# Optimization experiments

Hardware: AMD Instinct MI355X
Metric: run time of the kernel (lower is better)

## Reference

```python
import jax, jax.numpy as jnp
import numpy as np

DM, NE, ES, ESZ = 1024, 16, 4, 64  # dm, nexperts, expertsets, expertsize (dff = NE*ES*ESZ = 4096)
BATCH, SEQ = 8, 2048


def setup_inputs() -> dict:
    key = jax.random.key(0)
    k = jax.random.split(key, 5)
    scale = 0.02
    return {
        "x": jax.random.normal(k[0], (BATCH, SEQ, DM), dtype=jnp.float32),
        "controller": jax.random.normal(k[1], (DM, NE, ES), dtype=jnp.float32) * scale,
        "f1": jax.random.normal(k[2], (DM, NE, ES, ESZ), dtype=jnp.float32) * scale,
        "f2": jax.random.normal(k[3], (NE, ES, ESZ, DM), dtype=jnp.float32) * scale,
        "bias": jax.random.normal(k[4], (NE, ES, ESZ), dtype=jnp.float32) * scale,
    }


def reference(x, controller, f1, f2, bias):
    ne = controller.shape[1]
    d = x.shape[-1]
    # group tokens: [..., (b t), d] -> [..., b, t, d] with t = nexperts
    grouped = x.reshape(x.shape[:-2] + (-1, ne, d))
    # controller logits per token/expert/expertset: [..., b, t, e, s]
    logits = jnp.einsum('...btd,des->...btes', grouped, controller)
    # deterministic tiebreaker over the token-within-group axis t
    tie = jnp.linspace(0.0, 1e-6, ne, dtype=logits.dtype).reshape(ne, 1, 1)
    logits = logits + tie
    # hard top-1 permutation: for each (e, s) pick the argmax token t (one-hot over t)
    perm = (logits == jnp.max(logits, axis=-3, keepdims=True)).astype(x.dtype)
    # dispatch: select the chosen token's activations per (e, s): [..., b, e, s, d]
    sel = jnp.einsum('...btd,...btes->...besd', grouped, perm)
    # expert FFN up-projection + bias + relu: [..., b, e, s, f]
    inner = jax.nn.relu(jnp.einsum('...besd,desf->...besf', sel, f1) + bias)
    # expert FFN down-projection: [..., b, e, s, d]
    inter = jnp.einsum('...besf,esfd->...besd', inner, f2)
    # un-permute back to token positions: [..., b, t, d]
    out = jnp.einsum('...besd,...btes->...btd', inter, perm)
    return out.reshape(x.shape)
```

## Files before the change

kernel.cpp:

```cpp
#include <hip/hip_runtime.h>

#define DM   1024
#define NES  64
#define ESZ  64
#define NG   1024
#define TOK  16

typedef __bf16 bf16;
typedef __bf16 bf16x4 __attribute__((ext_vector_type(4)));
typedef __bf16 bf16x8 __attribute__((ext_vector_type(8)));
typedef float  f32x4  __attribute__((ext_vector_type(4)));

__device__ __forceinline__ void gld_lds16(const bf16* g, bf16* s) {
    __builtin_amdgcn_global_load_lds(
        (const __attribute__((address_space(1))) void*)g,
        (__attribute__((address_space(3))) void*)s, 16, 0, 0);
}

__global__ __launch_bounds__(256) void k0_transpose(const float* __restrict__ f1,
                                                    const float* __restrict__ f2,
                                                    bf16* __restrict__ f1p,
                                                    bf16* __restrict__ f2t) {
    __shared__ float tile[64 * 65];
    const int es = blockIdx.y, d0 = blockIdx.x * 64, tid = threadIdx.x;
    #pragma unroll
    for (int i = 0; i < 4; ++i) {
        int idx = i * 256 + tid; int r = idx >> 4, c4 = (idx & 15) * 4;
        float4 v = *(const float4*)(f1 + (size_t)(d0 + r) * 4096 + es * 64 + c4);
        tile[r * 65 + c4] = v.x; tile[r * 65 + c4 + 1] = v.y;
        tile[r * 65 + c4 + 2] = v.z; tile[r * 65 + c4 + 3] = v.w;
    }
    __syncthreads();
    #pragma unroll
    for (int i = 0; i < 2; ++i) {
        int idx = i * 256 + tid; int f = idx >> 3, dl0 = (idx & 7) * 8;
        bf16x8 o;
        #pragma unroll
        for (int j = 0; j < 8; ++j) o[j] = (bf16)tile[(dl0 + j) * 65 + f];
        *(bf16x8*)(f1p + (size_t)es * 65536 + f * 1024 + d0 + dl0) = o;
    }
    __syncthreads();
    #pragma unroll
    for (int i = 0; i < 4; ++i) {
        int idx = i * 256 + tid; int r = idx >> 4, c4 = (idx & 15) * 4;
        float4 v = *(const float4*)(f2 + (size_t)es * 65536 + r * 1024 + d0 + c4);
        tile[r * 65 + c4] = v.x; tile[r * 65 + c4 + 1] = v.y;
        tile[r * 65 + c4 + 2] = v.z; tile[r * 65 + c4 + 3] = v.w;
    }
    __syncthreads();
    #pragma unroll
    for (int i = 0; i < 2; ++i) {
        int idx = i * 256 + tid; int dl = idx >> 3, f0 = (idx & 7) * 8;
        bf16x8 o;
        #pragma unroll
        for (int j = 0; j < 8; ++j) o[j] = (bf16)tile[(f0 + j) * 65 + dl];
        *(bf16x8*)(f2t + (size_t)es * 65536 + (size_t)(d0 + dl) * 64 + f0) = o;
    }
}

__global__ __launch_bounds__(256) void k1_logits(const float* __restrict__ x,
                                                 const float* __restrict__ ctrl,
                                                 int* __restrict__ sel,
                                                 unsigned* __restrict__ selp) {
    __shared__ __align__(16) float xs[TOK * 132];
    __shared__ float sl[TOK * NES];
    __shared__ int   st[NES];
    const int bg  = blockIdx.x;
    const int tid = threadIdx.x;
    const int es  = tid & 63;
    const int tq  = tid >> 6;
    const float* xg = x + (size_t)bg * (TOK * DM);
    const float* cp = ctrl + es;
    float acc[4] = {0.f, 0.f, 0.f, 0.f};
    for (int d0 = 0; d0 < DM; d0 += 128) {
        __syncthreads();
        #pragma unroll
        for (int c = 0; c < 2; ++c) {
            int idx = tid + c * 256;
            int tr  = idx >> 5;
            int c4  = (idx & 31) * 4;
            float4 v = *(const float4*)(xg + tr * DM + d0 + c4);
            *(float4*)(xs + tr * 132 + c4) = v;
        }
        __syncthreads();
        #pragma unroll 2
        for (int dl4 = 0; dl4 < 128; dl4 += 4) {
            float4 v0 = *(const float4*)(xs + (tq * 4 + 0) * 132 + dl4);
            float4 v1 = *(const float4*)(xs + (tq * 4 + 1) * 132 + dl4);
            float4 v2 = *(const float4*)(xs + (tq * 4 + 2) * 132 + dl4);
            float4 v3 = *(const float4*)(xs + (tq * 4 + 3) * 132 + dl4);
            float c0 = cp[(size_t)(d0 + dl4 + 0) * 64];
            float c1 = cp[(size_t)(d0 + dl4 + 1) * 64];
            float c2 = cp[(size_t)(d0 + dl4 + 2) * 64];
            float c3 = cp[(size_t)(d0 + dl4 + 3) * 64];
            acc[0] += v0.x * c0; acc[1] += v1.x * c0;
            acc[2] += v2.x * c0; acc[3] += v3.x * c0;
            acc[0] += v0.y * c1; acc[1] += v1.y * c1;
            acc[2] += v2.y * c1; acc[3] += v3.y * c1;
            acc[0] += v0.z * c2; acc[1] += v1.z * c2;
            acc[2] += v2.z * c2; acc[3] += v3.z * c2;
            acc[0] += v0.w * c3; acc[1] += v1.w * c3;
            acc[2] += v2.w * c3; acc[3] += v3.w * c3;
        }
    }
    #pragma unroll
    for (int i = 0; i < 4; ++i) {
        int t = tq * 4 + i;
        sl[t * NES + es] = acc[i] + (float)t * (1e-6f / 15.f);
    }
    __syncthreads();
    if (tid < NES) {
        float best = -1e30f; int bi = 0;
        #pragma unroll
        for (int t = 0; t < TOK; ++t) {
            float v = sl[t * NES + tid];
            if (v >= best) { best = v; bi = t; }
        }
        sel[bg * NES + tid] = bi;
        st[tid] = bi;
    }
    __syncthreads();
    if (tid < 8) {
        unsigned p = 0;
        #pragma unroll
        for (int k = 0; k < 8; ++k) p |= (unsigned)st[tid * 8 + k] << (4 * k);
        selp[bg * 8 + tid] = p;
    }
}

__global__ __launch_bounds__(256) void k2_ffn1(const float* __restrict__ x,
                                               const bf16* __restrict__ f1p,
                                               const float* __restrict__ bias,
                                               const int* __restrict__ sel,
                                               bf16* __restrict__ inner) {
    __shared__ int  sel_s[128];
    __shared__ __align__(16) bf16 As[128 * 40];
    __shared__ __align__(16) bf16 Bs[64 * 40];
    const int es  = blockIdx.y;
    const int g0  = blockIdx.x * 128;
    const int tid = threadIdx.x;
    if (tid < 128) sel_s[tid] = sel[(g0 + tid) * 64 + es];
    __syncthreads();

    const int w = tid >> 6, l = tid & 63, quad = l >> 4, lr = l & 15;
    int tokrow[4];
    #pragma unroll
    for (int p = 0; p < 4; ++p) {
        int grow = p * 32 + (tid >> 3);
        tokrow[p] = (g0 + grow) * 16 + sel_s[grow];
    }
    const int c4 = (tid & 7) * 4;
    const int bf = tid >> 2, bd = (tid & 3) * 8;
    const bf16* f1es = f1p + (size_t)es * (DM * ESZ);

    f32x4 acc[2][4];
    #pragma unroll
    for (int mt = 0; mt < 2; ++mt)
        #pragma unroll
        for (int nt = 0; nt < 4; ++nt)
            acc[mt][nt] = (f32x4){0.f, 0.f, 0.f, 0.f};

    for (int k0 = 0; k0 < DM; k0 += 32) {
        #pragma unroll
        for (int p = 0; p < 4; ++p) {
            int grow = p * 32 + (tid >> 3);
            float4 v = *(const float4*)(x + (size_t)tokrow[p] * DM + k0 + c4);
            bf16x4 ob = {(bf16)v.x, (bf16)v.y, (bf16)v.z, (bf16)v.w};
            *(bf16x4*)(As + grow * 40 + c4) = ob;
        }
        {
            bf16x8 v = *(const bf16x8*)(f1es + bf * 1024 + k0 + bd);
            *(bf16x8*)(Bs + bf * 40 + bd) = v;
        }
        __syncthreads();
        bf16x8 av[2], bv[4];
        #pragma unroll
        for (int mt = 0; mt < 2; ++mt)
            av[mt] = *(const bf16x8*)(As + (w * 32 + mt * 16 + lr) * 40 + quad * 8);
        #pragma unroll
        for (int nt = 0; nt < 4; ++nt)
            bv[nt] = *(const bf16x8*)(Bs + (nt * 16 + lr) * 40 + quad * 8);
        #pragma unroll
        for (int mt = 0; mt < 2; ++mt)
            #pragma unroll
            for (int nt = 0; nt < 4; ++nt)
                acc[mt][nt] = __builtin_amdgcn_mfma_f32_16x16x32_bf16(
                    av[mt], bv[nt], acc[mt][nt], 0, 0, 0);
        __syncthreads();
    }
    bf16* innes = inner + (size_t)es * (NG * ESZ);
    #pragma unroll
    for (int mt = 0; mt < 2; ++mt)
        #pragma unroll
        for (int nt = 0; nt < 4; ++nt) {
            int f = nt * 16 + lr;
            float b = bias[es * 64 + f];
            #pragma unroll
            for (int r = 0; r < 4; ++r) {
                int grow = w * 32 + mt * 16 + quad * 4 + r;
                float v = acc[mt][nt][r] + b;
                v = v > 0.f ? v : 0.f;
                innes[(size_t)(g0 + grow) * 64 + f] = (bf16)v;
            }
        }
}

__global__ __launch_bounds__(256) void k3_ffn2(const bf16* __restrict__ inner,
                                               const bf16* __restrict__ f2t,
                                               const unsigned* __restrict__ selp,
                                               float* __restrict__ out) {
    __shared__ float accs[512 * 32];
    __shared__ __align__(16) bf16 As[2][32 * 64];
    __shared__ __align__(16) bf16 Bs[2][32 * 64];
    const int d0  = blockIdx.x * 32;
    const int g0  = blockIdx.y * 32;
    const int tid = threadIdx.x;
    const int w = tid >> 6, l = tid & 63, quad = l >> 4, lr = l & 15;
    const int mh = w >> 1, nh = w & 1;

    unsigned sp[4][8];
    #pragma unroll
    for (int r = 0; r < 4; ++r) {
        int gl = mh * 16 + quad * 4 + r;
        uint4 a = *(const uint4*)(selp + (size_t)(g0 + gl) * 8);
        uint4 b = *(const uint4*)(selp + (size_t)(g0 + gl) * 8 + 4);
        sp[r][0] = a.x; sp[r][1] = a.y; sp[r][2] = a.z; sp[r][3] = a.w;
        sp[r][4] = b.x; sp[r][5] = b.y; sp[r][6] = b.z; sp[r][7] = b.w;
    }

    const int srow = tid >> 3;
    const int scb  = ((tid & 7) * 16) ^ ((srow & 7) << 4);
    const bf16* srcA = inner + (size_t)(g0 + srow) * 64 + (scb >> 1);
    const bf16* srcB = f2t   + (size_t)(d0 + srow) * 64 + (scb >> 1);
    bf16* dA0 = &As[0][w * 512]; bf16* dA1 = &As[1][w * 512];
    bf16* dB0 = &Bs[0][w * 512]; bf16* dB1 = &Bs[1][w * 512];

    #pragma unroll
    for (int i = 0; i < 16; ++i)
        ((f32x4*)accs)[i * 256 + tid] = (f32x4){0.f, 0.f, 0.f, 0.f};

    gld_lds16(srcA, dA0);
    gld_lds16(srcB, dB0);
    __syncthreads();

    const int rowA = mh * 16 + lr, rowB = nh * 16 + lr;
    const int offA0 = rowA * 128 + ((quad * 16)      ^ ((rowA & 7) << 4));
    const int offA1 = rowA * 128 + ((quad * 16 + 64) ^ ((rowA & 7) << 4));
    const int offB0 = rowB * 128 + ((quad * 16)      ^ ((rowB & 7) << 4));
    const int offB1 = rowB * 128 + ((quad * 16 + 64) ^ ((rowB & 7) << 4));

    #pragma unroll
    for (int es = 0; es < 64; ++es) {
        const int cur = es & 1;
        if (es < 63) {
            if (cur == 0) { gld_lds16(srcA + (size_t)(es + 1) * 65536, dA1);
                            gld_lds16(srcB + (size_t)(es + 1) * 65536, dB1); }
            else          { gld_lds16(srcA + (size_t)(es + 1) * 65536, dA0);
                            gld_lds16(srcB + (size_t)(es + 1) * 65536, dB0); }
            asm volatile("s_waitcnt vmcnt(2)" ::: "memory");
        } else {
            asm volatile("s_waitcnt vmcnt(0)" ::: "memory");
        }
        asm volatile("s_barrier" ::: "memory");

        const char* a = (const char*)As[cur];
        const char* b = (const char*)Bs[cur];
        bf16x8 a0 = *(const bf16x8*)(a + offA0);
        bf16x8 a1 = *(const bf16x8*)(a + offA1);
        bf16x8 b0 = *(const bf16x8*)(b + offB0);
        bf16x8 b1 = *(const bf16x8*)(b + offB1);
        f32x4 z = {0.f, 0.f, 0.f, 0.f};
        z = __builtin_amdgcn_mfma_f32_16x16x32_bf16(a0, b0, z, 0, 0, 0);
        z = __builtin_amdgcn_mfma_f32_16x16x32_bf16(a1, b1, z, 0, 0, 0);

        const int dw = es >> 3, sh = (es & 7) * 4;
        #pragma unroll
        for (int r = 0; r < 4; ++r) {
            int t    = (sp[r][dw] >> sh) & 15;
            int gl   = mh * 16 + quad * 4 + r;
            int scol = (nh * 16 + lr) ^ ((t & 7) << 2);
            accs[(gl * 16 + t) * 32 + scol] += z[r];
        }
        asm volatile("s_barrier" ::: "memory");
    }
    __syncthreads();
    #pragma unroll
    for (int i = 0; i < 16; ++i) {
        int fi = i * 256 + tid;
        int row = fi >> 3, q = fi & 7;
        int scol4 = (q * 4) ^ ((row & 7) << 2);
        f32x4 v = *(f32x4*)(accs + row * 32 + scol4);
        __builtin_nontemporal_store(v, (f32x4*)(out + (size_t)(g0 * 16 + row) * DM + d0 + q * 4));
    }
}

extern "C" void kernel_launch(void* const* d_in, const int* in_sizes, int n_in,
                              void* d_out, int out_size, void* d_ws, size_t ws_size,
                              hipStream_t stream) {
    const float* x    = (const float*)d_in[0];
    const float* ctrl = (const float*)d_in[1];
    const float* f1   = (const float*)d_in[2];
    const float* f2   = (const float*)d_in[3];
    const float* bias = (const float*)d_in[4];
    float* out = (float*)d_out;

    char* ws = (char*)d_ws;
    bf16*     f1p   = (bf16*)(ws);
    bf16*     f2t   = (bf16*)(ws + 8388608);
    bf16*     inner = (bf16*)(ws + 16777216);
    int*      sel   = (int*)(ws + 25165824);
    unsigned* selp  = (unsigned*)(ws + 25427968);

    hipLaunchKernelGGL(k0_transpose, dim3(16, 64), dim3(256), 0, stream, f1, f2, f1p, f2t);
    hipLaunchKernelGGL(k1_logits,    dim3(1024),   dim3(256), 0, stream, x, ctrl, sel, selp);
    hipLaunchKernelGGL(k2_ffn1,      dim3(8, 64),  dim3(256), 0, stream, x, f1p, bias, sel, inner);
    hipLaunchKernelGGL(k3_ffn2,      dim3(32, 32), dim3(256), 0, stream, inner, f2t, selp, out);
}
```

Before: 306.1 us.

## Emit bf16 x copy from logits kernel, stage controller in LDS, prefetch ffn1 tiles

The logits kernel now stages controller chunks in shared memory instead of issuing strided global loads per thread. It prefetches the next x and controller chunk into registers while computing the current one. When the workspace is large enough, it also writes a bf16 copy of x, so the ffn1 gather reads half the bytes and skips conversion. The ffn1 kernel switches to 64-row tiles with register prefetch of the next k-slice, doubling the grid. This adds an extra 32MB write in k1 and depends on workspace size.

```diff
diff --git a/kernel.cpp b/kernel.cpp
--- a/kernel.cpp
+++ b/kernel.cpp
@@ -58,11 +58,14 @@
     }
 }
 
+template<int WRITE_XB>
 __global__ __launch_bounds__(256) void k1_logits(const float* __restrict__ x,
                                                  const float* __restrict__ ctrl,
                                                  int* __restrict__ sel,
-                                                 unsigned* __restrict__ selp) {
-    __shared__ __align__(16) float xs[TOK * 132];
+                                                 unsigned* __restrict__ selp,
+                                                 bf16* __restrict__ xb) {
+    __shared__ __align__(16) float xs[TOK * 64];
+    __shared__ __align__(16) float cs[64 * 64];
     __shared__ float sl[TOK * NES];
     __shared__ int   st[NES];
     const int bg  = blockIdx.x;
@@ -70,29 +73,45 @@
     const int es  = tid & 63;
     const int tq  = tid >> 6;
     const float* xg = x + (size_t)bg * (TOK * DM);
-    const float* cp = ctrl + es;
+    const int xr = tid >> 4, xc = (tid & 15) * 4;
     float acc[4] = {0.f, 0.f, 0.f, 0.f};
-    for (int d0 = 0; d0 < DM; d0 += 128) {
+
+    float4 xv;
+    float4 cv[4];
+    xv = *(const float4*)(xg + xr * DM + xc);
+    #pragma unroll
+    for (int j = 0; j < 4; ++j)
+        cv[j] = *(const float4*)(ctrl + (size_t)(tid + j * 256) * 4);
+
+    for (int c = 0; c < 16; ++c) {
+        const int d0 = c * 64;
         __syncthreads();
-        #pragma unroll
-        for (int c = 0; c < 2; ++c) {
-            int idx = tid + c * 256;
-            int tr  = idx >> 5;
-            int c4  = (idx & 31) * 4;
-            float4 v = *(const float4*)(xg + tr * DM + d0 + c4);
-            *(float4*)(xs + tr * 132 + c4) = v;
-        }
+        *(float4*)(xs + xr * 64 + xc) = xv;
+        if (WRITE_XB) {
+            bf16x4 o = {(bf16)xv.x, (bf16)xv.y, (bf16)xv.z, (bf16)xv.w};
+            *(bf16x4*)(xb + (size_t)(bg * TOK + xr) * DM + d0 + xc) = o;
+        }
+        #pragma unroll
+        for (int j = 0; j < 4; ++j)
+            *(float4*)(cs + tid * 4 + j * 1024) = cv[j];
         __syncthreads();
-        #pragma unroll 2
-        for (int dl4 = 0; dl4 < 128; dl4 += 4) {
-            float4 v0 = *(const float4*)(xs + (tq * 4 + 0) * 132 + dl4);
-            float4 v1 = *(const float4*)(xs + (tq * 4 + 1) * 132 + dl4);
-            float4 v2 = *(const float4*)(xs + (tq * 4 + 2) * 132 + dl4);
-            float4 v3 = *(const float4*)(xs + (tq * 4 + 3) * 132 + dl4);
-            float c0 = cp[(size_t)(d0 + dl4 + 0) * 64];
-            float c1 = cp[(size_t)(d0 + dl4 + 1) * 64];
-            float c2 = cp[(size_t)(d0 + dl4 + 2) * 64];
-            float c3 = cp[(size_t)(d0 + dl4 + 3) * 64];
+        if (c < 15) {
+            xv = *(const float4*)(xg + xr * DM + d0 + 64 + xc);
+            #pragma unroll
+            for (int j = 0; j < 4; ++j)
+                cv[j] = *(const float4*)(ctrl + (size_t)(d0 + 64) * 64 +
+                                         (size_t)(tid + j * 256) * 4);
+        }
+        #pragma unroll
+        for (int dl4 = 0; dl4 < 64; dl4 += 4) {
+            float4 v0 = *(const float4*)(xs + (tq * 4 + 0) * 64 + dl4);
+            float4 v1 = *(const float4*)(xs + (tq * 4 + 1) * 64 + dl4);
+            float4 v2 = *(const float4*)(xs + (tq * 4 + 2) * 64 + dl4);
+            float4 v3 = *(const float4*)(xs + (tq * 4 + 3) * 64 + dl4);
+            float c0 = cs[(dl4 + 0) * 64 + es];
+            float c1 = cs[(dl4 + 1) * 64 + es];
+            float c2 = cs[(dl4 + 2) * 64 + es];
+            float c3 = cs[(dl4 + 3) * 64 + es];
             acc[0] += v0.x * c0; acc[1] += v1.x * c0;
             acc[2] += v2.x * c0; acc[3] += v3.x * c0;
             acc[0] += v0.y * c1; acc[1] += v1.y * c1;
@@ -128,81 +147,92 @@
     }
 }
 
+template<int USE_XB>
 __global__ __launch_bounds__(256) void k2_ffn1(const float* __restrict__ x,
+                                               const bf16* __restrict__ xb,
                                                const bf16* __restrict__ f1p,
                                                const float* __restrict__ bias,
                                                const int* __restrict__ sel,
                                                bf16* __restrict__ inner) {
-    __shared__ int  sel_s[128];
-    __shared__ __align__(16) bf16 As[128 * 40];
+    __shared__ int  sel_s[64];
+    __shared__ __align__(16) bf16 As[64 * 40];
     __shared__ __align__(16) bf16 Bs[64 * 40];
     const int es  = blockIdx.y;
-    const int g0  = blockIdx.x * 128;
+    const int g0  = blockIdx.x * 64;
     const int tid = threadIdx.x;
-    if (tid < 128) sel_s[tid] = sel[(g0 + tid) * 64 + es];
+    if (tid < 64) sel_s[tid] = sel[(size_t)(g0 + tid) * 64 + es];
     __syncthreads();
 
     const int w = tid >> 6, l = tid & 63, quad = l >> 4, lr = l & 15;
-    int tokrow[4];
-    #pragma unroll
-    for (int p = 0; p < 4; ++p) {
-        int grow = p * 32 + (tid >> 3);
-        tokrow[p] = (g0 + grow) * 16 + sel_s[grow];
-    }
-    const int c4 = (tid & 7) * 4;
-    const int bf = tid >> 2, bd = (tid & 3) * 8;
+    const int rowq = tid >> 2, colq = (tid & 3) * 8;
+    const int row8 = tid >> 3, c4 = (tid & 7) * 4;
     const bf16* f1es = f1p + (size_t)es * (DM * ESZ);
 
-    f32x4 acc[2][4];
-    #pragma unroll
-    for (int mt = 0; mt < 2; ++mt)
-        #pragma unroll
-        for (int nt = 0; nt < 4; ++nt)
-            acc[mt][nt] = (f32x4){0.f, 0.f, 0.f, 0.f};
+    int tokq = 0, tok0 = 0, tok1 = 0;
+    if (USE_XB) {
+        tokq = (g0 + rowq) * 16 + sel_s[rowq];
+    } else {
+        tok0 = (g0 + row8) * 16 + sel_s[row8];
+        tok1 = (g0 + 32 + row8) * 16 + sel_s[32 + row8];
+    }
+
+    bf16x8 ra, rb;
+    float4 r0, r1;
+    if (USE_XB) {
+        ra = *(const bf16x8*)(xb + (size_t)tokq * DM + colq);
+    } else {
+        r0 = *(const float4*)(x + (size_t)tok0 * DM + c4);
+        r1 = *(const float4*)(x + (size_t)tok1 * DM + c4);
+    }
+    rb = *(const bf16x8*)(f1es + rowq * 1024 + colq);
+
+    f32x4 acc[4];
+    #pragma unroll
+    for (int nt = 0; nt < 4; ++nt) acc[nt] = (f32x4){0.f, 0.f, 0.f, 0.f};
 
     for (int k0 = 0; k0 < DM; k0 += 32) {
-        #pragma unroll
-        for (int p = 0; p < 4; ++p) {
-            int grow = p * 32 + (tid >> 3);
-            float4 v = *(const float4*)(x + (size_t)tokrow[p] * DM + k0 + c4);
-            bf16x4 ob = {(bf16)v.x, (bf16)v.y, (bf16)v.z, (bf16)v.w};
-            *(bf16x4*)(As + grow * 40 + c4) = ob;
-        }
-        {
-            bf16x8 v = *(const bf16x8*)(f1es + bf * 1024 + k0 + bd);
-            *(bf16x8*)(Bs + bf * 40 + bd) = v;
-        }
+        if (USE_XB) {
+            *(bf16x8*)(As + rowq * 40 + colq) = ra;
+        } else {
+            bf16x4 o0 = {(bf16)r0.x, (bf16)r0.y, (bf16)r0.z, (bf16)r0.w};
+            bf16x4 o1 = {(bf16)r1.x, (bf16)r1.y, (bf16)r1.z, (bf16)r1.w};
+            *(bf16x4*)(As + row8 * 40 + c4) = o0;
+            *(bf16x4*)(As + (32 + row8) * 40 + c4) = o1;
+        }
+        *(bf16x8*)(Bs + rowq * 40 + colq) = rb;
         __syncthreads();
-        bf16x8 av[2], bv[4];
-        #pragma unroll
-        for (int mt = 0; mt < 2; ++mt)
-            av[mt] = *(const bf16x8*)(As + (w * 32 + mt * 16 + lr) * 40 + quad * 8);
+        if (k0 + 32 < DM) {
+            if (USE_XB) {
+                ra = *(const bf16x8*)(xb + (size_t)tokq * DM + k0 + 32 + colq);
+            } else {
+                r0 = *(const float4*)(x + (size_t)tok0 * DM + k0 + 32 + c4);
+                r1 = *(const float4*)(x + (size_t)tok1 * DM + k0 + 32 + c4);
+            }
+            rb = *(const bf16x8*)(f1es + rowq * 1024 + k0 + 32 + colq);
+        }
+        bf16x8 av = *(const bf16x8*)(As + (w * 16 + lr) * 40 + quad * 8);
+        bf16x8 bv[4];
         #pragma unroll
         for (int nt = 0; nt < 4; ++nt)
             bv[nt] = *(const bf16x8*)(Bs + (nt * 16 + lr) * 40 + quad * 8);
         #pragma unroll
-        for (int mt = 0; mt < 2; ++mt)
-            #pragma unroll
-            for (int nt = 0; nt < 4; ++nt)
-                acc[mt][nt] = __builtin_amdgcn_mfma_f32_16x16x32_bf16(
-                    av[mt], bv[nt], acc[mt][nt], 0, 0, 0);
+        for (int nt = 0; nt < 4; ++nt)
+            acc[nt] = __builtin_amdgcn_mfma_f32_16x16x32_bf16(av, bv[nt], acc[nt], 0, 0, 0);
         __syncthreads();
     }
     bf16* innes = inner + (size_t)es * (NG * ESZ);
     #pragma unroll
-    for (int mt = 0; mt < 2; ++mt)
-        #pragma unroll
-        for (int nt = 0; nt < 4; ++nt) {
-            int f = nt * 16 + lr;
-            float b = bias[es * 64 + f];
-            #pragma unroll
-            for (int r = 0; r < 4; ++r) {
-                int grow = w * 32 + mt * 16 + quad * 4 + r;
-                float v = acc[mt][nt][r] + b;
-                v = v > 0.f ? v : 0.f;
-                innes[(size_t)(g0 + grow) * 64 + f] = (bf16)v;
-            }
-        }
+    for (int nt = 0; nt < 4; ++nt) {
+        int f = nt * 16 + lr;
+        float b = bias[es * 64 + f];
+        #pragma unroll
+        for (int r = 0; r < 4; ++r) {
+            int grow = w * 16 + quad * 4 + r;
+            float v = acc[nt][r] + b;
+            v = v > 0.f ? v : 0.f;
+            innes[(size_t)(g0 + grow) * 64 + f] = (bf16)v;
+        }
+    }
 }
 
 __global__ __launch_bounds__(256) void k3_ffn2(const bf16* __restrict__ inner,
@@ -310,9 +340,18 @@
     bf16*     inner = (bf16*)(ws + 16777216);
     int*      sel   = (int*)(ws + 25165824);
     unsigned* selp  = (unsigned*)(ws + 25427968);
+    bf16*     xb    = (bf16*)(ws + 25460736);
+
+    const size_t need_xb = (size_t)25460736 + (size_t)NG * TOK * DM * sizeof(bf16);
+    const bool use_xb = ws_size >= need_xb;
 
     hipLaunchKernelGGL(k0_transpose, dim3(16, 64), dim3(256), 0, stream, f1, f2, f1p, f2t);
-    hipLaunchKernelGGL(k1_logits,    dim3(1024),   dim3(256), 0, stream, x, ctrl, sel, selp);
-    hipLaunchKernelGGL(k2_ffn1,      dim3(8, 64),  dim3(256), 0, stream, x, f1p, bias, sel, inner);
-    hipLaunchKernelGGL(k3_ffn2,      dim3(32, 32), dim3(256), 0, stream, inner, f2t, selp, out);
-}
+    if (use_xb) {
+        hipLaunchKernelGGL((k1_logits<1>), dim3(1024), dim3(256), 0, stream, x, ctrl, sel, selp, xb);
+        hipLaunchKernelGGL((k2_ffn1<1>),   dim3(16, 64), dim3(256), 0, stream, x, xb, f1p, bias, sel, inner);
+    } else {
+        hipLaunchKernelGGL((k1_logits<0>), dim3(1024), dim3(256), 0, stream, x, ctrl, sel, selp, xb);
+        hipLaunchKernelGGL((k2_ffn1<0>),   dim3(16, 64), dim3(256), 0, stream, x, xb, f1p, bias, sel, inner);
+    }
+    hipLaunchKernelGGL(k3_ffn2, dim3(32, 32), dim3(256), 0, stream, inner, f2t, selp, out);
+}
```

After: 342.8 us. 12.0% more time.

## Stage controller in LDS with register-prefetched chunks and 512-thread logits blocks

Applied to the files above, without the earlier changes.

The logits kernel now loads 64-wide chunks of both x and the controller into shared memory, prefetching the next chunk into registers while the current one is computed. The block grows to 512 threads, each accumulating 2 tokens instead of 4. This replaces strided per-thread global controller reads with coalesced loads reused from LDS, and overlaps global latency with compute. In exchange it adds more barriers per iteration and uses more shared memory per block.

```diff
diff --git a/kernel.cpp b/kernel.cpp
--- a/kernel.cpp
+++ b/kernel.cpp
@@ -58,11 +58,12 @@
     }
 }
 
-__global__ __launch_bounds__(256) void k1_logits(const float* __restrict__ x,
+__global__ __launch_bounds__(512) void k1_logits(const float* __restrict__ x,
                                                  const float* __restrict__ ctrl,
                                                  int* __restrict__ sel,
                                                  unsigned* __restrict__ selp) {
-    __shared__ __align__(16) float xs[TOK * 132];
+    __shared__ __align__(16) float xs[TOK * 64];
+    __shared__ __align__(16) float cs[64 * 64];
     __shared__ float sl[TOK * NES];
     __shared__ int   st[NES];
     const int bg  = blockIdx.x;
@@ -70,42 +71,48 @@
     const int es  = tid & 63;
     const int tq  = tid >> 6;
     const float* xg = x + (size_t)bg * (TOK * DM);
-    const float* cp = ctrl + es;
-    float acc[4] = {0.f, 0.f, 0.f, 0.f};
-    for (int d0 = 0; d0 < DM; d0 += 128) {
+    const int xr = tid >> 4, xc = (tid & 15) * 4;
+    float acc[2] = {0.f, 0.f};
+
+    float4 xv;
+    float4 cv[2];
+    if (tid < 256) xv = *(const float4*)(xg + xr * DM + xc);
+    #pragma unroll
+    for (int j = 0; j < 2; ++j)
+        cv[j] = *(const float4*)(ctrl + (size_t)(tid + j * 512) * 4);
+
+    for (int c = 0; c < 16; ++c) {
+        const int d0 = c * 64;
         __syncthreads();
-        #pragma unroll
-        for (int c = 0; c < 2; ++c) {
-            int idx = tid + c * 256;
-            int tr  = idx >> 5;
-            int c4  = (idx & 31) * 4;
-            float4 v = *(const float4*)(xg + tr * DM + d0 + c4);
-            *(float4*)(xs + tr * 132 + c4) = v;
-        }
+        if (tid < 256) *(float4*)(xs + xr * 64 + xc) = xv;
+        #pragma unroll
+        for (int j = 0; j < 2; ++j)
+            *(float4*)(cs + (size_t)(tid + j * 512) * 4) = cv[j];
         __syncthreads();
-        #pragma unroll 2
-        for (int dl4 = 0; dl4 < 128; dl4 += 4) {
-            float4 v0 = *(const float4*)(xs + (tq * 4 + 0) * 132 + dl4);
-            float4 v1 = *(const float4*)(xs + (tq * 4 + 1) * 132 + dl4);
-            float4 v2 = *(const float4*)(xs + (tq * 4 + 2) * 132 + dl4);
-            float4 v3 = *(const float4*)(xs + (tq * 4 + 3) * 132 + dl4);
-            float c0 = cp[(size_t)(d0 + dl4 + 0) * 64];
-            float c1 = cp[(size_t)(d0 + dl4 + 1) * 64];
-            float c2 = cp[(size_t)(d0 + dl4 + 2) * 64];
-            float c3 = cp[(size_t)(d0 + dl4 + 3) * 64];
+        if (c < 15) {
+            if (tid < 256) xv = *(const float4*)(xg + xr * DM + d0 + 64 + xc);
+            #pragma unroll
+            for (int j = 0; j < 2; ++j)
+                cv[j] = *(const float4*)(ctrl + (size_t)(d0 + 64) * 64 +
+                                         (size_t)(tid + j * 512) * 4);
+        }
+        #pragma unroll
+        for (int dl4 = 0; dl4 < 64; dl4 += 4) {
+            float4 v0 = *(const float4*)(xs + (tq * 2 + 0) * 64 + dl4);
+            float4 v1 = *(const float4*)(xs + (tq * 2 + 1) * 64 + dl4);
+            float c0 = cs[(dl4 + 0) * 64 + es];
+            float c1 = cs[(dl4 + 1) * 64 + es];
+            float c2 = cs[(dl4 + 2) * 64 + es];
+            float c3 = cs[(dl4 + 3) * 64 + es];
             acc[0] += v0.x * c0; acc[1] += v1.x * c0;
-            acc[2] += v2.x * c0; acc[3] += v3.x * c0;
             acc[0] += v0.y * c1; acc[1] += v1.y * c1;
-            acc[2] += v2.y * c1; acc[3] += v3.y * c1;
             acc[0] += v0.z * c2; acc[1] += v1.z * c2;
-            acc[2] += v2.z * c2; acc[3] += v3.z * c2;
             acc[0] += v0.w * c3; acc[1] += v1.w * c3;
-            acc[2] += v2.w * c3; acc[3] += v3.w * c3;
-        }
-    }
-    #pragma unroll
-    for (int i = 0; i < 4; ++i) {
-        int t = tq * 4 + i;
+        }
+    }
+    #pragma unroll
+    for (int i = 0; i < 2; ++i) {
+        int t = tq * 2 + i;
         sl[t * NES + es] = acc[i] + (float)t * (1e-6f / 15.f);
     }
     __syncthreads();
@@ -312,7 +319,7 @@
     unsigned* selp  = (unsigned*)(ws + 25427968);
 
     hipLaunchKernelGGL(k0_transpose, dim3(16, 64), dim3(256), 0, stream, f1, f2, f1p, f2t);
-    hipLaunchKernelGGL(k1_logits,    dim3(1024),   dim3(256), 0, stream, x, ctrl, sel, selp);
+    hipLaunchKernelGGL(k1_logits,    dim3(1024),   dim3(512), 0, stream, x, ctrl, sel, selp);
     hipLaunchKernelGGL(k2_ffn1,      dim3(8, 64),  dim3(256), 0, stream, x, f1p, bias, sel, inner);
     hipLaunchKernelGGL(k3_ffn2,      dim3(32, 32), dim3(256), 0, stream, inner, f2t, selp, out);
 }
```

Result: slower. 343.5 us (+12.2%).

## Load ffn1 MFMA operands directly from global memory, dropping LDS staging

Applied to the files above, without the earlier changes.

The ffn1 kernel no longer stages x and f1 tiles through shared memory with two barriers per k-step. Each lane now loads its MFMA A and B fragments straight from global memory (x rows gathered via sel, f1 rows) and converts x to bf16 in registers, with the k loop unrolled by 4. This removes the LDS writes, the barriers and the LDS reads. In exchange, f1 fragments are re-read by all four waves and the global accesses are less coalesced, so cache traffic rises.

```diff
diff --git a/kernel.cpp b/kernel.cpp
--- a/kernel.cpp
+++ b/kernel.cpp
@@ -133,25 +133,22 @@
                                                const float* __restrict__ bias,
                                                const int* __restrict__ sel,
                                                bf16* __restrict__ inner) {
-    __shared__ int  sel_s[128];
-    __shared__ __align__(16) bf16 As[128 * 40];
-    __shared__ __align__(16) bf16 Bs[64 * 40];
     const int es  = blockIdx.y;
     const int g0  = blockIdx.x * 128;
     const int tid = threadIdx.x;
-    if (tid < 128) sel_s[tid] = sel[(g0 + tid) * 64 + es];
-    __syncthreads();
-
     const int w = tid >> 6, l = tid & 63, quad = l >> 4, lr = l & 15;
-    int tokrow[4];
-    #pragma unroll
-    for (int p = 0; p < 4; ++p) {
-        int grow = p * 32 + (tid >> 3);
-        tokrow[p] = (g0 + grow) * 16 + sel_s[grow];
-    }
-    const int c4 = (tid & 7) * 4;
-    const int bf = tid >> 2, bd = (tid & 3) * 8;
     const bf16* f1es = f1p + (size_t)es * (DM * ESZ);
+
+    const int grow0 = w * 32 + lr;
+    const int grow1 = w * 32 + 16 + lr;
+    const int tok0 = (g0 + grow0) * 16 + sel[(size_t)(g0 + grow0) * 64 + es];
+    const int tok1 = (g0 + grow1) * 16 + sel[(size_t)(g0 + grow1) * 64 + es];
+    const float* xa0 = x + (size_t)tok0 * DM + quad * 8;
+    const float* xa1 = x + (size_t)tok1 * DM + quad * 8;
+    const bf16* fb0 = f1es + (size_t)(0 * 16 + lr) * 1024 + quad * 8;
+    const bf16* fb1 = f1es + (size_t)(1 * 16 + lr) * 1024 + quad * 8;
+    const bf16* fb2 = f1es + (size_t)(2 * 16 + lr) * 1024 + quad * 8;
+    const bf16* fb3 = f1es + (size_t)(3 * 16 + lr) * 1024 + quad * 8;
 
     f32x4 acc[2][4];
     #pragma unroll
@@ -160,34 +157,30 @@
         for (int nt = 0; nt < 4; ++nt)
             acc[mt][nt] = (f32x4){0.f, 0.f, 0.f, 0.f};
 
+    #pragma unroll 4
     for (int k0 = 0; k0 < DM; k0 += 32) {
-        #pragma unroll
-        for (int p = 0; p < 4; ++p) {
-            int grow = p * 32 + (tid >> 3);
-            float4 v = *(const float4*)(x + (size_t)tokrow[p] * DM + k0 + c4);
-            bf16x4 ob = {(bf16)v.x, (bf16)v.y, (bf16)v.z, (bf16)v.w};
-            *(bf16x4*)(As + grow * 40 + c4) = ob;
-        }
-        {
-            bf16x8 v = *(const bf16x8*)(f1es + bf * 1024 + k0 + bd);
-            *(bf16x8*)(Bs + bf * 40 + bd) = v;
-        }
-        __syncthreads();
-        bf16x8 av[2], bv[4];
-        #pragma unroll
-        for (int mt = 0; mt < 2; ++mt)
-            av[mt] = *(const bf16x8*)(As + (w * 32 + mt * 16 + lr) * 40 + quad * 8);
-        #pragma unroll
-        for (int nt = 0; nt < 4; ++nt)
-            bv[nt] = *(const bf16x8*)(Bs + (nt * 16 + lr) * 40 + quad * 8);
-        #pragma unroll
-        for (int mt = 0; mt < 2; ++mt)
-            #pragma unroll
-            for (int nt = 0; nt < 4; ++nt)
-                acc[mt][nt] = __builtin_amdgcn_mfma_f32_16x16x32_bf16(
-                    av[mt], bv[nt], acc[mt][nt], 0, 0, 0);
-        __syncthreads();
-    }
+        float4 a0l = *(const float4*)(xa0 + k0);
+        float4 a0h = *(const float4*)(xa0 + k0 + 4);
+        float4 a1l = *(const float4*)(xa1 + k0);
+        float4 a1h = *(const float4*)(xa1 + k0 + 4);
+        bf16x8 bv0 = *(const bf16x8*)(fb0 + k0);
+        bf16x8 bv1 = *(const bf16x8*)(fb1 + k0);
+        bf16x8 bv2 = *(const bf16x8*)(fb2 + k0);
+        bf16x8 bv3 = *(const bf16x8*)(fb3 + k0);
+        bf16x8 av0 = {(bf16)a0l.x, (bf16)a0l.y, (bf16)a0l.z, (bf16)a0l.w,
+                      (bf16)a0h.x, (bf16)a0h.y, (bf16)a0h.z, (bf16)a0h.w};
+        bf16x8 av1 = {(bf16)a1l.x, (bf16)a1l.y, (bf16)a1l.z, (bf16)a1l.w,
+                      (bf16)a1h.x, (bf16)a1h.y, (bf16)a1h.z, (bf16)a1h.w};
+        acc[0][0] = __builtin_amdgcn_mfma_f32_16x16x32_bf16(av0, bv0, acc[0][0], 0, 0, 0);
+        acc[0][1] = __builtin_amdgcn_mfma_f32_16x16x32_bf16(av0, bv1, acc[0][1], 0, 0, 0);
+        acc[0][2] = __builtin_amdgcn_mfma_f32_16x16x32_bf16(av0, bv2, acc[0][2], 0, 0, 0);
+        acc[0][3] = __builtin_amdgcn_mfma_f32_16x16x32_bf16(av0, bv3, acc[0][3], 0, 0, 0);
+        acc[1][0] = __builtin_amdgcn_mfma_f32_16x16x32_bf16(av1, bv0, acc[1][0], 0, 0, 0);
+        acc[1][1] = __builtin_amdgcn_mfma_f32_16x16x32_bf16(av1, bv1, acc[1][1], 0, 0, 0);
+        acc[1][2] = __builtin_amdgcn_mfma_f32_16x16x32_bf16(av1, bv2, acc[1][2], 0, 0, 0);
+        acc[1][3] = __builtin_amdgcn_mfma_f32_16x16x32_bf16(av1, bv3, acc[1][3], 0, 0, 0);
+    }
+
     bf16* innes = inner + (size_t)es * (NG * ESZ);
     #pragma unroll
     for (int mt = 0; mt < 2; ++mt)
```

Result: slower. 336.7 us (+10.0%).
